# Optimization experiments

Hardware: AMD Instinct MI355X
Metric: run time of the kernel (lower is better)

Reference implementation:

```python
import jax, jax.numpy as jnp
import numpy as np

N = 50000        # nodes
E = 800000       # edges
F_IN = 128       # input_nf == output_nf
HID = 128        # hidden_nf
HEADS = 4
HD = HID // HEADS            # 32 per-head hidden
FEAT = 2 * F_IN + 1 + 1 + 1 + 9   # 268 edge feature dim


def setup_inputs() -> dict:
    key = jax.random.key(0)
    ks = jax.random.split(key, 16)
    f32 = jnp.float32
    inp = {}
    inp["h"] = jax.random.normal(ks[0], (N, F_IN), dtype=f32)
    inp["coord"] = jax.random.normal(ks[1], (N, 3), dtype=f32)
    inp["edge_index"] = jax.random.randint(ks[2], (2, E), 0, N, dtype=jnp.int64 if jax.config.read('jax_enable_x64') else jnp.int32)
    # per-head edge MLP: Linear(FEAT,HD) -> SiLU -> Linear(HD,HD), stacked over heads
    inp["eW1"] = jax.random.normal(ks[3], (HEADS, FEAT, HD), dtype=f32) / np.sqrt(FEAT)
    inp["eb1"] = jnp.zeros((HEADS, HD), dtype=f32)
    inp["eW2"] = jax.random.normal(ks[4], (HEADS, HD, HD), dtype=f32) / np.sqrt(HD)
    inp["eb2"] = jnp.zeros((HEADS, HD), dtype=f32)
    # LayerNorm over hidden_nf
    inp["ln_g"] = jnp.ones((HID,), dtype=f32)
    inp["ln_b"] = jnp.zeros((HID,), dtype=f32)
    # node_mlp: Linear(HID+F_IN, HID) -> SiLU -> Linear(HID, F_IN)
    inp["nW1"] = jax.random.normal(ks[5], (HID + F_IN, HID), dtype=f32) / np.sqrt(HID + F_IN)
    inp["nb1"] = jnp.zeros((HID,), dtype=f32)
    inp["nW2"] = jax.random.normal(ks[6], (HID, F_IN), dtype=f32) / np.sqrt(HID)
    inp["nb2"] = jnp.zeros((F_IN,), dtype=f32)
    # coord_mlp: Linear(HID, HID) -> SiLU -> Linear(HID, 1, bias=False, xavier gain=0.001)
    inp["cW1"] = jax.random.normal(ks[7], (HID, HID), dtype=f32) / np.sqrt(HID)
    inp["cb1"] = jnp.zeros((HID,), dtype=f32)
    inp["cW2"] = jax.random.normal(ks[8], (HID, 1), dtype=f32) * 0.001
    return inp


def _forward(h, coord, edge_index, eW1, eb1, eW2, eb2, ln_g, ln_b,
             nW1, nb1, nW2, nb2, cW1, cb1, cW2):
    eps, thr = 1e-8, 1e-6
    row, col = edge_index[0], edge_index[1]
    n = h.shape[0]
    ci = coord[row]            # [E,3]
    ck = coord[col]            # [E,3]
    coord_diff = ci - ck       # rel_coord, also used for coord update
    radial = jnp.sum(coord_diff * coord_diff, axis=-1, keepdims=True)   # [E,1]
    dist = jnp.sqrt(radial)                                             # ||rel_coord||
    dot = jnp.sum(ci * ck, axis=-1, keepdims=True)                      # [E,1]
    # SO3 frame per edge
    a = coord_diff / (jnp.linalg.norm(coord_diff, axis=1, keepdims=True) + eps)
    cp = jnp.cross(ci, ck)
    b = cp / (jnp.linalg.norm(cp, axis=1, keepdims=True) + eps)
    c = jnp.cross(a, b)
    mask = ((jnp.linalg.norm(a, axis=1) < thr) |
            (jnp.linalg.norm(b, axis=1) < thr) |
            (jnp.linalg.norm(c, axis=1) < thr))
    so3 = jnp.stack([a, b, c], axis=2)                                  # [E,3,3] columns a,b,c
    so3 = jnp.where(mask[:, None, None], jnp.eye(3, dtype=so3.dtype), so3)
    so3_flat = so3.reshape(-1, 9)
    # edge features -> per-head small MLPs
    feats = jnp.concatenate([h[row], h[col], radial, dist, dot, so3_flat], axis=1)  # [E,FEAT]
    x = jax.nn.silu(jnp.einsum('ef,hfd->hed', feats, eW1) + eb1[:, None, :])
    x = jnp.einsum('hed,hdk->hek', x, eW2) + eb2[:, None, :]            # [H,E,HD]
    edge_feat = jnp.transpose(x, (1, 0, 2)).reshape(x.shape[1], -1)     # [E,HID], head-major concat
    # LayerNorm
    mu = edge_feat.mean(axis=-1, keepdims=True)
    var = edge_feat.var(axis=-1, keepdims=True)
    edge_feat = (edge_feat - mu) / jnp.sqrt(var + 1e-5) * ln_g + ln_b
    # coord update
    w = jax.nn.silu(edge_feat @ cW1 + cb1) @ cW2                        # [E,1]
    trans = coord_diff * w
    coord_out = coord + jax.ops.segment_sum(trans, row, num_segments=n)
    # node update
    agg = jax.ops.segment_sum(edge_feat, row, num_segments=n)           # [N,HID]
    y = jax.nn.silu(jnp.concatenate([h, agg], axis=1) @ nW1 + nb1) @ nW2 + nb2
    h_out = h + y                                                       # residual
    return h_out, coord_out


def reference(h, coord, edge_index, eW1, eb1, eW2, eb2, ln_g, ln_b,
              nW1, nb1, nW2, nb2, cW1, cb1, cW2):
    return _forward(h, coord, edge_index, eW1, eb1, eW2, eb2, ln_g, ln_b,
                    nW1, nb1, nW2, nb2, cW1, cb1, cW2)
```

## Files before the change

### kernel.cpp

```cpp
#include <hip/hip_runtime.h>
#include <hip/hip_bf16.h>
#include <math.h>

#define NN 50000
#define EE 800000
#define FIN 128
#define HIDN 128
#define HD 32
#define FEATD 268
#define K1 288
#define KP1 296
#define TE 64
#define TN2 64

typedef __bf16 bf16x8 __attribute__((ext_vector_type(8)));
typedef __bf16 bf16x4 __attribute__((ext_vector_type(4)));
typedef float  f32x4  __attribute__((ext_vector_type(4)));

#define MFMA(a, b, c) __builtin_amdgcn_mfma_f32_16x16x32_bf16((a), (b), (c), 0, 0, 0)

__device__ __forceinline__ float silu_f(float x) {
    return x / (1.0f + __expf(-x));
}

__global__ void wconv_kernel(const float* __restrict__ eW1, const float* __restrict__ eW2,
                             const float* __restrict__ cW1, const float* __restrict__ nW1,
                             const float* __restrict__ nW2,
                             __bf16* __restrict__ eW1t, __bf16* __restrict__ eW2t,
                             __bf16* __restrict__ cW1t, __bf16* __restrict__ nW1t,
                             __bf16* __restrict__ nW2t)
{
    const int i = blockIdx.x * 256 + threadIdx.x;
    if (i < 4 * 32 * K1) {
        const int hh = i / (32 * K1), rs = i % (32 * K1), d = rs / K1, k = rs % K1;
        const float v = (k < FEATD) ? eW1[(size_t)hh * FEATD * HD + (size_t)k * HD + d] : 0.f;
        eW1t[i] = (__bf16)v;
    }
    if (i < 4 * HD * HD) {
        const int hh = i / (HD * HD), rs = i % (HD * HD), d = rs / HD, k = rs % HD;
        eW2t[i] = (__bf16)eW2[(size_t)hh * HD * HD + (size_t)k * HD + d];
    }
    if (i < HIDN * HIDN) {
        const int o = i / HIDN, k = i % HIDN;
        cW1t[i] = (__bf16)cW1[(size_t)k * HIDN + o];
    }
    if (i < HIDN * (2 * FIN)) {
        const int o = i / (2 * FIN), k = i % (2 * FIN);
        nW1t[i] = (__bf16)nW1[(size_t)k * HIDN + o];
    }
    if (i < FIN * HIDN) {
        const int o = i / HIDN, k = i % HIDN;
        nW2t[i] = (__bf16)nW2[(size_t)k * FIN + o];
    }
}

__global__ __launch_bounds__(512) void edge_kernel(
    const float* __restrict__ h, const float* __restrict__ coord,
    const int* __restrict__ ei,
    const __bf16* __restrict__ eW1t, const float* __restrict__ eb1,
    const __bf16* __restrict__ eW2t, const float* __restrict__ eb2,
    const float* __restrict__ ln_g, const float* __restrict__ ln_b,
    const __bf16* __restrict__ cW1t, const float* __restrict__ cb1,
    const float* __restrict__ cW2,
    float* __restrict__ houtbase, float* __restrict__ coord_out)
{
    __shared__ __align__(16) unsigned char smemA[TE * KP1 * 2];
    __shared__ __align__(16) unsigned char smemB[4 * TE * 40 * 2];
    __shared__ float cdiff[TE][3];
    __shared__ int   rowlds[TE];
    __shared__ float wsum[TE];

    __bf16 (*featsB)[KP1] = (__bf16 (*)[KP1])smemA;
    float  (*efs)[132]    = (float  (*)[132])smemA;
    __bf16 (*efsB)[136]   = (__bf16 (*)[136])smemB;

    const int t  = threadIdx.x;
    const int e0 = blockIdx.x * TE;

    if (t < TE) wsum[t] = 0.f;

    {
        const int e = t >> 3;
        const int q = t & 7;
        const int r = ei[e0 + e];
        const int c = ei[EE + e0 + e];
        const float4* hr = (const float4*)(h + (size_t)r * FIN);
        const float4* hc = (const float4*)(h + (size_t)c * FIN);
        #pragma unroll
        for (int j = 0; j < 4; j++) {
            const int f4 = q + 8 * j;
            float4 v = hr[f4];
            bf16x4 bv = { (__bf16)v.x, (__bf16)v.y, (__bf16)v.z, (__bf16)v.w };
            *(bf16x4*)&featsB[e][f4 * 4] = bv;
            float4 u = hc[f4];
            bf16x4 bu = { (__bf16)u.x, (__bf16)u.y, (__bf16)u.z, (__bf16)u.w };
            *(bf16x4*)&featsB[e][FIN + f4 * 4] = bu;
        }
        if (q == 0) {
            rowlds[e] = r;
            const float cix = coord[(size_t)r*3+0], ciy = coord[(size_t)r*3+1], ciz = coord[(size_t)r*3+2];
            const float ckx = coord[(size_t)c*3+0], cky = coord[(size_t)c*3+1], ckz = coord[(size_t)c*3+2];
            const float dx = cix-ckx, dy = ciy-cky, dz = ciz-ckz;
            cdiff[e][0]=dx; cdiff[e][1]=dy; cdiff[e][2]=dz;
            const float radial = dx*dx + dy*dy + dz*dz;
            const float dist   = sqrtf(radial);
            const float dotv   = cix*ckx + ciy*cky + ciz*ckz;
            const float ia = 1.0f / (dist + 1e-8f);
            float ax = dx*ia, ay = dy*ia, az = dz*ia;
            const float cpx = ciy*ckz - ciz*cky;
            const float cpy = ciz*ckx - cix*ckz;
            const float cpz = cix*cky - ciy*ckx;
            const float cpn = sqrtf(cpx*cpx + cpy*cpy + cpz*cpz);
            const float ib = 1.0f / (cpn + 1e-8f);
            float bx = cpx*ib, by = cpy*ib, bz = cpz*ib;
            float cx = ay*bz - az*by;
            float cy = az*bx - ax*bz;
            float cz = ax*by - ay*bx;
            const float na = sqrtf(ax*ax + ay*ay + az*az);
            const float nb = sqrtf(bx*bx + by*by + bz*bz);
            const float nc = sqrtf(cx*cx + cy*cy + cz*cz);
            if (na < 1e-6f || nb < 1e-6f || nc < 1e-6f) {
                ax=1.f; bx=0.f; cx=0.f;
                ay=0.f; by=1.f; cy=0.f;
                az=0.f; bz=0.f; cz=1.f;
            }
            featsB[e][256]=(__bf16)radial; featsB[e][257]=(__bf16)dist; featsB[e][258]=(__bf16)dotv;
            featsB[e][259]=(__bf16)ax; featsB[e][260]=(__bf16)bx; featsB[e][261]=(__bf16)cx;
            featsB[e][262]=(__bf16)ay; featsB[e][263]=(__bf16)by; featsB[e][264]=(__bf16)cy;
            featsB[e][265]=(__bf16)az; featsB[e][266]=(__bf16)bz; featsB[e][267]=(__bf16)cz;
            #pragma unroll
            for (int k = FEATD; k < K1; k++) featsB[e][k] = (__bf16)0.f;
        }
    }
    __syncthreads();

    const int wv2  = t >> 6;
    const int hh   = wv2 >> 1;
    const int mh   = wv2 & 1;
    const int lane = t & 63;
    const int lr   = lane & 15;
    const int lg   = lane >> 4;

    __bf16* hidB = ((__bf16*)smemB) + hh * (TE * 40);

    const f32x4 z4 = { 0.f, 0.f, 0.f, 0.f };

    {
        f32x4 acc[2][2];
        #pragma unroll
        for (int mti = 0; mti < 2; mti++) { acc[mti][0] = z4; acc[mti][1] = z4; }
        const __bf16* W1 = eW1t + (size_t)hh * 32 * K1;
        #pragma unroll
        for (int ks = 0; ks < 9; ks++) {
            const int kof = ks * 32 + lg * 8;
            bf16x8 b0 = *(const bf16x8*)(W1 + (size_t)lr * K1 + kof);
            bf16x8 b1 = *(const bf16x8*)(W1 + (size_t)(16 + lr) * K1 + kof);
            #pragma unroll
            for (int mti = 0; mti < 2; mti++) {
                bf16x8 a = *(const bf16x8*)(&featsB[(mh * 2 + mti) * 16 + lr][kof]);
                acc[mti][0] = MFMA(a, b0, acc[mti][0]);
                acc[mti][1] = MFMA(a, b1, acc[mti][1]);
            }
        }
        const float b1a = eb1[hh * HD + lr];
        const float b1b = eb1[hh * HD + 16 + lr];
        #pragma unroll
        for (int mti = 0; mti < 2; mti++) {
            #pragma unroll
            for (int r = 0; r < 4; r++) {
                const int erow = (mh * 2 + mti) * 16 + lg * 4 + r;
                hidB[erow * 40 + lr]      = (__bf16)silu_f(acc[mti][0][r] + b1a);
                hidB[erow * 40 + 16 + lr] = (__bf16)silu_f(acc[mti][1][r] + b1b);
            }
        }
    }
    __syncthreads();

    {
        f32x4 acc2[2][2];
        #pragma unroll
        for (int mti = 0; mti < 2; mti++) { acc2[mti][0] = z4; acc2[mti][1] = z4; }
        const __bf16* W2 = eW2t + (size_t)hh * HD * HD;
        const int kof2 = lg * 8;
        bf16x8 b20 = *(const bf16x8*)(W2 + (size_t)lr * HD + kof2);
        bf16x8 b21 = *(const bf16x8*)(W2 + (size_t)(16 + lr) * HD + kof2);
        #pragma unroll
        for (int mti = 0; mti < 2; mti++) {
            bf16x8 a = *(const bf16x8*)(hidB + ((mh * 2 + mti) * 16 + lr) * 40 + kof2);
            acc2[mti][0] = MFMA(a, b20, acc2[mti][0]);
            acc2[mti][1] = MFMA(a, b21, acc2[mti][1]);
        }
        const float b2a = eb2[hh * HD + lr];
        const float b2b = eb2[hh * HD + 16 + lr];
        #pragma unroll
        for (int mti = 0; mti < 2; mti++) {
            #pragma unroll
            for (int r = 0; r < 4; r++) {
                const int erow = (mh * 2 + mti) * 16 + lg * 4 + r;
                efs[erow][hh * HD + lr]      = acc2[mti][0][r] + b2a;
                efs[erow][hh * HD + 16 + lr] = acc2[mti][1][r] + b2b;
            }
        }
    }
    __syncthreads();

    {
        const int el = t >> 3;
        const int q8 = t & 7;
        float s = 0.f, s2 = 0.f;
        #pragma unroll
        for (int i = 0; i < 16; i++) {
            const float v = efs[el][q8 + 8 * i];
            s += v; s2 += v * v;
        }
        s  += __shfl_xor(s, 1);  s  += __shfl_xor(s, 2);  s  += __shfl_xor(s, 4);
        s2 += __shfl_xor(s2, 1); s2 += __shfl_xor(s2, 2); s2 += __shfl_xor(s2, 4);
        const float mu   = s * (1.f / 128.f);
        const float var  = s2 * (1.f / 128.f) - mu * mu;
        const float rstd = rsqrtf(var + 1e-5f);
        #pragma unroll
        for (int i = 0; i < 16; i++) {
            const int oo = q8 + 8 * i;
            const float v  = efs[el][oo];
            const float nv = (v - mu) * rstd * ln_g[oo] + ln_b[oo];
            efs[el][oo]  = nv;
            efsB[el][oo] = (__bf16)nv;
        }
    }
    __syncthreads();

    {
        f32x4 acc3[2][2];
        #pragma unroll
        for (int mti = 0; mti < 2; mti++) { acc3[mti][0] = z4; acc3[mti][1] = z4; }
        const __bf16* W3 = cW1t + (size_t)hh * 32 * HIDN;
        #pragma unroll
        for (int ks = 0; ks < 4; ks++) {
            const int kof = ks * 32 + lg * 8;
            bf16x8 b30 = *(const bf16x8*)(W3 + (size_t)lr * HIDN + kof);
            bf16x8 b31 = *(const bf16x8*)(W3 + (size_t)(16 + lr) * HIDN + kof);
            #pragma unroll
            for (int mti = 0; mti < 2; mti++) {
                bf16x8 a = *(const bf16x8*)(&efsB[(mh * 2 + mti) * 16 + lr][kof]);
                acc3[mti][0] = MFMA(a, b30, acc3[mti][0]);
                acc3[mti][1] = MFMA(a, b31, acc3[mti][1]);
            }
        }
        const int c0 = hh * 32 + lr, c1 = c0 + 16;
        const float cbA = cb1[c0], cbB = cb1[c1];
        const float cwA = cW2[c0], cwB = cW2[c1];
        float pe[8];
        #pragma unroll
        for (int mti = 0; mti < 2; mti++)
            #pragma unroll
            for (int r = 0; r < 4; r++)
                pe[mti * 4 + r] = silu_f(acc3[mti][0][r] + cbA) * cwA
                                + silu_f(acc3[mti][1][r] + cbB) * cwB;
        #pragma unroll
        for (int d = 1; d < 16; d <<= 1)
            #pragma unroll
            for (int i = 0; i < 8; i++) pe[i] += __shfl_xor(pe[i], d);
        if (lr == 0) {
            #pragma unroll
            for (int mti = 0; mti < 2; mti++)
                #pragma unroll
                for (int r = 0; r < 4; r++)
                    atomicAdd(&wsum[(mh * 2 + mti) * 16 + lg * 4 + r], pe[mti * 4 + r]);
        }
    }
    __syncthreads();

    if (t < TE) {
        const float we = wsum[t];
        const int r = rowlds[t];
        atomicAdd(&coord_out[(size_t)r*3+0], cdiff[t][0] * we);
        atomicAdd(&coord_out[(size_t)r*3+1], cdiff[t][1] * we);
        atomicAdd(&coord_out[(size_t)r*3+2], cdiff[t][2] * we);
    }

    {
        const int p  = t & 63;
        const int gq = t >> 6;
        #pragma unroll
        for (int e2 = 0; e2 < 8; e2++) {
            const int ee = gq * 8 + e2;
            const float lo = efs[ee][2 * p];
            const float hi = efs[ee][2 * p + 1];
            __hip_bfloat162 pk;
            pk.x = __float2bfloat16(lo);
            pk.y = __float2bfloat16(hi);
            __hip_bfloat162* addr = (__hip_bfloat162*)
                ((char*)houtbase + (size_t)rowlds[ee] * 512 + 256 + p * 4);
            unsafeAtomicAdd(addr, pk);
        }
    }
}

__global__ __launch_bounds__(512) void node_kernel(
    const float* __restrict__ h,
    const __bf16* __restrict__ nW1t, const float* __restrict__ nb1,
    const __bf16* __restrict__ nW2t, const float* __restrict__ nb2,
    float* __restrict__ h_out)
{
    __shared__ __align__(16) __bf16 featsN[TN2][264];
    __shared__ __align__(16) __bf16 hidN[TN2][136];

    const int t  = threadIdx.x;
    const int n0 = blockIdx.x * TN2;

    {
        const int n = t >> 3;
        const int q = t & 7;
        const int nid = n0 + n;
        const bool ok = nid < NN;
        const float4* hr = (const float4*)(h + (size_t)nid * FIN);
        #pragma unroll
        for (int j = 0; j < 4; j++) {
            const int f4 = q + 8 * j;
            float4 v = ok ? hr[f4] : make_float4(0.f, 0.f, 0.f, 0.f);
            bf16x4 bv = { (__bf16)v.x, (__bf16)v.y, (__bf16)v.z, (__bf16)v.w };
            *(bf16x4*)&featsN[n][f4 * 4] = bv;
        }
        const uint4* ar = (const uint4*)((const char*)h_out + (size_t)nid * 512 + 256);
        #pragma unroll
        for (int j = 0; j < 2; j++) {
            const int w4 = q * 2 + j;
            uint4 u = ok ? ar[w4] : make_uint4(0u, 0u, 0u, 0u);
            *(uint4*)&featsN[n][FIN + w4 * 8] = u;
        }
    }
    __syncthreads();

    const int wv2  = t >> 6;
    const int hh2  = wv2 >> 1;
    const int mh   = wv2 & 1;
    const int lane = t & 63;
    const int lr   = lane & 15;
    const int lg   = lane >> 4;

    const f32x4 z4 = { 0.f, 0.f, 0.f, 0.f };

    {
        f32x4 acc[2][2];
        #pragma unroll
        for (int mti = 0; mti < 2; mti++) { acc[mti][0] = z4; acc[mti][1] = z4; }
        const __bf16* W1 = nW1t + (size_t)hh2 * 32 * 256;
        #pragma unroll
        for (int ks = 0; ks < 8; ks++) {
            const int kof = ks * 32 + lg * 8;
            bf16x8 b0 = *(const bf16x8*)(W1 + (size_t)lr * 256 + kof);
            bf16x8 b1 = *(const bf16x8*)(W1 + (size_t)(16 + lr) * 256 + kof);
            #pragma unroll
            for (int mti = 0; mti < 2; mti++) {
                bf16x8 a = *(const bf16x8*)(&featsN[(mh * 2 + mti) * 16 + lr][kof]);
                acc[mti][0] = MFMA(a, b0, acc[mti][0]);
                acc[mti][1] = MFMA(a, b1, acc[mti][1]);
            }
        }
        const float b1a = nb1[hh2 * 32 + lr];
        const float b1b = nb1[hh2 * 32 + 16 + lr];
        #pragma unroll
        for (int mti = 0; mti < 2; mti++) {
            #pragma unroll
            for (int r = 0; r < 4; r++) {
                const int erow = (mh * 2 + mti) * 16 + lg * 4 + r;
                hidN[erow][hh2 * 32 + lr]      = (__bf16)silu_f(acc[mti][0][r] + b1a);
                hidN[erow][hh2 * 32 + 16 + lr] = (__bf16)silu_f(acc[mti][1][r] + b1b);
            }
        }
    }
    __syncthreads();

    {
        f32x4 acc2[2][2];
        #pragma unroll
        for (int mti = 0; mti < 2; mti++) { acc2[mti][0] = z4; acc2[mti][1] = z4; }
        const __bf16* W2 = nW2t + (size_t)hh2 * 32 * 128;
        #pragma unroll
        for (int ks = 0; ks < 4; ks++) {
            const int kof = ks * 32 + lg * 8;
            bf16x8 b0 = *(const bf16x8*)(W2 + (size_t)lr * 128 + kof);
            bf16x8 b1 = *(const bf16x8*)(W2 + (size_t)(16 + lr) * 128 + kof);
            #pragma unroll
            for (int mti = 0; mti < 2; mti++) {
                bf16x8 a = *(const bf16x8*)(&hidN[(mh * 2 + mti) * 16 + lr][kof]);
                acc2[mti][0] = MFMA(a, b0, acc2[mti][0]);
                acc2[mti][1] = MFMA(a, b1, acc2[mti][1]);
            }
        }
        const float b2a = nb2[hh2 * 32 + lr];
        const float b2b = nb2[hh2 * 32 + 16 + lr];
        const int c0 = hh2 * 32 + lr, c1 = c0 + 16;
        #pragma unroll
        for (int mti = 0; mti < 2; mti++) {
            #pragma unroll
            for (int r = 0; r < 4; r++) {
                const int erow = (mh * 2 + mti) * 16 + lg * 4 + r;
                const int nid  = n0 + erow;
                if (nid < NN) {
                    h_out[(size_t)nid * FIN + c0] = h[(size_t)nid * FIN + c0] + acc2[mti][0][r] + b2a;
                    h_out[(size_t)nid * FIN + c1] = h[(size_t)nid * FIN + c1] + acc2[mti][1][r] + b2b;
                }
            }
        }
    }
}

extern "C" void kernel_launch(void* const* d_in, const int* in_sizes, int n_in,
                              void* d_out, int out_size, void* d_ws, size_t ws_size,
                              hipStream_t stream)
{
    (void)in_sizes; (void)n_in; (void)out_size; (void)ws_size;
    const float* h     = (const float*)d_in[0];
    const float* coord = (const float*)d_in[1];
    const int*   ei    = (const int*)d_in[2];
    const float* eW1   = (const float*)d_in[3];
    const float* eb1   = (const float*)d_in[4];
    const float* eW2   = (const float*)d_in[5];
    const float* eb2   = (const float*)d_in[6];
    const float* ln_g  = (const float*)d_in[7];
    const float* ln_b  = (const float*)d_in[8];
    const float* nW1   = (const float*)d_in[9];
    const float* nb1   = (const float*)d_in[10];
    const float* nW2   = (const float*)d_in[11];
    const float* nb2   = (const float*)d_in[12];
    const float* cW1   = (const float*)d_in[13];
    const float* cb1   = (const float*)d_in[14];
    const float* cW2   = (const float*)d_in[15];

    float* h_out     = (float*)d_out;
    float* coord_out = h_out + (size_t)NN * FIN;

    __bf16* eW1t = (__bf16*)d_ws;
    __bf16* eW2t = eW1t + 4 * 32 * K1;
    __bf16* cW1t = eW2t + 4 * HD * HD;
    __bf16* nW1t = cW1t + HIDN * HIDN;
    __bf16* nW2t = nW1t + HIDN * (2 * FIN);

    hipMemsetAsync(h_out, 0, (size_t)NN * FIN * sizeof(float), stream);
    hipMemcpyAsync(coord_out, coord, (size_t)NN * 3 * sizeof(float),
                   hipMemcpyDeviceToDevice, stream);
    wconv_kernel<<<(4 * 32 * K1 + 255) / 256, 256, 0, stream>>>(
        eW1, eW2, cW1, nW1, nW2, eW1t, eW2t, cW1t, nW1t, nW2t);

    edge_kernel<<<EE / TE, 512, 0, stream>>>(h, coord, ei, eW1t, eb1, eW2t, eb2,
                                             ln_g, ln_b, cW1t, cb1, cW2,
                                             h_out, coord_out);
    node_kernel<<<(NN + TN2 - 1) / TN2, 512, 0, stream>>>(h, nW1t, nb1, nW2t, nb2, h_out);
}
```

Before: 456.9 us.

## Pre-convert h to bf16 in output scratch and gather bf16 rows in edge kernel

```diff
diff --git a/kernel.cpp b/kernel.cpp
--- a/kernel.cpp
+++ b/kernel.cpp
@@ -54,8 +54,22 @@
     }
 }
 
+__global__ __launch_bounds__(256) void hconv_kernel(const float* __restrict__ h,
+                                                    float* __restrict__ houtbase)
+{
+    const int i = blockIdx.x * 256 + threadIdx.x;
+    if (i >= NN * FIN / 8) return;
+    const int row = i >> 4;
+    const int c8  = i & 15;
+    const float4* src = (const float4*)(h + (size_t)row * FIN + c8 * 8);
+    float4 a = src[0], b = src[1];
+    bf16x8 v = { (__bf16)a.x, (__bf16)a.y, (__bf16)a.z, (__bf16)a.w,
+                 (__bf16)b.x, (__bf16)b.y, (__bf16)b.z, (__bf16)b.w };
+    *(bf16x8*)((char*)houtbase + (size_t)row * 512 + c8 * 16) = v;
+}
+
 __global__ __launch_bounds__(512) void edge_kernel(
-    const float* __restrict__ h, const float* __restrict__ coord,
+    const float* __restrict__ coord,
     const int* __restrict__ ei,
     const __bf16* __restrict__ eW1t, const float* __restrict__ eb1,
     const __bf16* __restrict__ eW2t, const float* __restrict__ eb2,
@@ -84,17 +98,13 @@
         const int q = t & 7;
         const int r = ei[e0 + e];
         const int c = ei[EE + e0 + e];
-        const float4* hr = (const float4*)(h + (size_t)r * FIN);
-        const float4* hc = (const float4*)(h + (size_t)c * FIN);
-        #pragma unroll
-        for (int j = 0; j < 4; j++) {
-            const int f4 = q + 8 * j;
-            float4 v = hr[f4];
-            bf16x4 bv = { (__bf16)v.x, (__bf16)v.y, (__bf16)v.z, (__bf16)v.w };
-            *(bf16x4*)&featsB[e][f4 * 4] = bv;
-            float4 u = hc[f4];
-            bf16x4 bu = { (__bf16)u.x, (__bf16)u.y, (__bf16)u.z, (__bf16)u.w };
-            *(bf16x4*)&featsB[e][FIN + f4 * 4] = bu;
+        #pragma unroll
+        for (int j = 0; j < 2; j++) {
+            const int c16 = q + 8 * j;
+            uint4 vr = *(const uint4*)((const char*)houtbase + (size_t)r * 512 + c16 * 16);
+            *(uint4*)&featsB[e][c16 * 8] = vr;
+            uint4 vc = *(const uint4*)((const char*)houtbase + (size_t)c * 512 + c16 * 16);
+            *(uint4*)&featsB[e][FIN + c16 * 8] = vc;
         }
         if (q == 0) {
             rowlds[e] = r;
@@ -223,7 +233,6 @@
             const int oo = q8 + 8 * i;
             const float v  = efs[el][oo];
             const float nv = (v - mu) * rstd * ln_g[oo] + ln_b[oo];
-            efs[el][oo]  = nv;
             efsB[el][oo] = (__bf16)nv;
         }
     }
@@ -284,11 +293,7 @@
         #pragma unroll
         for (int e2 = 0; e2 < 8; e2++) {
             const int ee = gq * 8 + e2;
-            const float lo = efs[ee][2 * p];
-            const float hi = efs[ee][2 * p + 1];
-            __hip_bfloat162 pk;
-            pk.x = __float2bfloat16(lo);
-            pk.y = __float2bfloat16(hi);
+            __hip_bfloat162 pk = *(__hip_bfloat162*)&efsB[ee][2 * p];
             __hip_bfloat162* addr = (__hip_bfloat162*)
                 ((char*)houtbase + (size_t)rowlds[ee] * 512 + 256 + p * 4);
             unsafeAtomicAdd(addr, pk);
@@ -313,20 +318,12 @@
         const int q = t & 7;
         const int nid = n0 + n;
         const bool ok = nid < NN;
-        const float4* hr = (const float4*)(h + (size_t)nid * FIN);
+        const uint4* rowp = (const uint4*)((const char*)h_out + (size_t)nid * 512);
         #pragma unroll
         for (int j = 0; j < 4; j++) {
-            const int f4 = q + 8 * j;
-            float4 v = ok ? hr[f4] : make_float4(0.f, 0.f, 0.f, 0.f);
-            bf16x4 bv = { (__bf16)v.x, (__bf16)v.y, (__bf16)v.z, (__bf16)v.w };
-            *(bf16x4*)&featsN[n][f4 * 4] = bv;
-        }
-        const uint4* ar = (const uint4*)((const char*)h_out + (size_t)nid * 512 + 256);
-        #pragma unroll
-        for (int j = 0; j < 2; j++) {
-            const int w4 = q * 2 + j;
-            uint4 u = ok ? ar[w4] : make_uint4(0u, 0u, 0u, 0u);
-            *(uint4*)&featsN[n][FIN + w4 * 8] = u;
+            const int w4 = q * 4 + j;
+            uint4 u = ok ? rowp[w4] : make_uint4(0u, 0u, 0u, 0u);
+            *(uint4*)&featsN[n][w4 * 8] = u;
         }
     }
     __syncthreads();
@@ -442,8 +439,9 @@
                    hipMemcpyDeviceToDevice, stream);
     wconv_kernel<<<(4 * 32 * K1 + 255) / 256, 256, 0, stream>>>(
         eW1, eW2, cW1, nW1, nW2, eW1t, eW2t, cW1t, nW1t, nW2t);
-
-    edge_kernel<<<EE / TE, 512, 0, stream>>>(h, coord, ei, eW1t, eb1, eW2t, eb2,
+    hconv_kernel<<<(NN * FIN / 8 + 255) / 256, 256, 0, stream>>>(h, h_out);
+
+    edge_kernel<<<EE / TE, 512, 0, stream>>>(coord, ei, eW1t, eb1, eW2t, eb2,
                                              ln_g, ln_b, cW1t, cb1, cW2,
                                              h_out, coord_out);
     node_kernel<<<(NN + TN2 - 1) / TN2, 512, 0, stream>>>(h, nW1t, nb1, nW2t, nb2, h_out);
```

New measurement: 435.6 us. 4.7% less time.
